# Kernel optimization log

Hardware: AMD Instinct MI355X
Metric: run time of the kernel (lower is better)

## Reference

```python
import jax, jax.numpy as jnp
import numpy as np

DN = ('NCHW', 'OIHW', 'NCHW')

def conv2d(x, w, b, stride, pad):
    y = jax.lax.conv_general_dilated(x, w, (stride, stride), [(pad, pad), (pad, pad)], dimension_numbers=DN)
    return y + b[None, :, None, None]

def conv_transpose2d(x, w, b):
    # torch ConvTranspose2d(k=4, stride=2, padding=1): out = (H-1)*2 - 2 + 4 = 2H
    # implemented as input-dilated conv with padding k-1-p = 2 on each side
    y = jax.lax.conv_general_dilated(x, w, (1, 1), [(2, 2), (2, 2)], lhs_dilation=(2, 2), dimension_numbers=DN)
    return y + b[None, :, None, None]

def setup_inputs() -> dict:
    key = jax.random.key(0)
    ks = jax.random.split(key, 8)
    K, D = 512, 128
    x = jax.random.normal(ks[0], (32, 3, 128, 128), jnp.float32)
    ew1 = jax.random.normal(ks[1], (128, 3, 4, 4), jnp.float32) * (1.0 / np.sqrt(3 * 16))
    eb1 = jnp.zeros((128,), jnp.float32)
    ew2 = jax.random.normal(ks[2], (D, 128, 4, 4), jnp.float32) * (1.0 / np.sqrt(128 * 16))
    eb2 = jnp.zeros((D,), jnp.float32)
    E = jax.random.uniform(ks[3], (K, D), jnp.float32, minval=-1.0 / K, maxval=1.0 / K)
    dw1 = jax.random.normal(ks[4], (128, D, 4, 4), jnp.float32) * (1.0 / np.sqrt(D * 16))
    db1 = jnp.zeros((128,), jnp.float32)
    dw2 = jax.random.normal(ks[5], (3, 128, 4, 4), jnp.float32) * (1.0 / np.sqrt(128 * 16))
    db2 = jnp.zeros((3,), jnp.float32)
    return {"x": x, "ew1": ew1, "eb1": eb1, "ew2": ew2, "eb2": eb2, "E": E,
            "dw1": dw1, "db1": db1, "dw2": dw2, "db2": db2}

def reference(x, ew1, eb1, ew2, eb2, E, dw1, db1, dw2, db2):
    # --- encoder: conv stack ---
    h = jax.nn.relu(conv2d(x, ew1, eb1, stride=2, pad=1))       # [B,128,64,64]
    z = conv2d(h, ew2, eb2, stride=2, pad=1)                    # [B,D,32,32] encoder_output
    B, C, H, W = z.shape
    Ze = jnp.transpose(z, (0, 2, 3, 1)).reshape(-1, C)          # [N_e, D], BHWC flattening
    # --- VQ: pairwise sq-dist, argmin, codebook lookup (== one-hot matmul in original) ---
    d = (jnp.sum(Ze * Ze, axis=1, keepdims=True)
         + jnp.sum(E * E, axis=1)
         - 2.0 * jnp.matmul(Ze, E.T))                           # [N_e, K]
    idx = jnp.argmin(d, axis=1)                                 # [N_e]
    Zq = E[idx]                                                 # [N_e, D]
    # faithful to original: Zq_mat.view(encoder_output.shape) with NO permute back
    dec_in = Zq.reshape(B, C, H, W)
    # straight-through estimator
    dec_in = z + jax.lax.stop_gradient(dec_in - z)
    # --- decoder: transposed conv stack ---
    g = jax.nn.relu(conv_transpose2d(dec_in, dw1, db1))         # [B,128,64,64]
    x_recon = jax.nn.sigmoid(conv_transpose2d(g, dw2, db2))     # [B,3,128,128]
    return x_recon
```

## Files before the change

### kernel.cpp

```cpp
#include <hip/hip_runtime.h>
#include <hip/hip_bf16.h>
#include <math.h>


typedef __attribute__((ext_vector_type(8))) short bf16x8;
typedef __attribute__((ext_vector_type(4))) float f32x4;

__device__ __forceinline__ void gload16(const void* g, const void* l) {
    __builtin_amdgcn_global_load_lds(
        (const __attribute__((address_space(1))) void*)g,
        (__attribute__((address_space(3))) void*)l, 16, 0, 0);
}

__device__ __forceinline__ int fragoff(int row, int ks, int lane) {
    return (row << 8) + (((ks << 6) + (lane & 0x30)) ^ ((row & 7) << 4));
}
__device__ __forceinline__ int fragoff64(int row, int ks, int lane) {
    return (row << 7) + (((ks << 6) + (lane & 0x30)) ^ ((row & 7) << 4));
}

__global__ __launch_bounds__(256) void k_init(
    const float* __restrict__ ew1, const float* __restrict__ ew2,
    const float* __restrict__ E,   const float* __restrict__ dw1,
    const float* __restrict__ dw2,
    __hip_bfloat16* __restrict__ hb,  __hip_bfloat16* __restrict__ w2p,
    __hip_bfloat16* __restrict__ w1p, __hip_bfloat16* __restrict__ Ep,
    __hip_bfloat16* __restrict__ w1b, __hip_bfloat16* __restrict__ w2db9,
    __hip_bfloat16* __restrict__ dq,  float* __restrict__ s2)
{
    int bid = blockIdx.x, t = threadIdx.x;
    bf16x8 zero8 = {0, 0, 0, 0, 0, 0, 0, 0};
    if (bid < 520) {
        int vid = bid * 256 + t;
        const int NROWV = 67584;
        if (vid < NROWV) {
            int c8 = (vid & 15) << 3;
            int xx = (vid >> 4) % 66;
            int r2 = vid / (66 * 16);
            int yy = (r2 & 1) * 65;
            int n = r2 >> 1;
            *(bf16x8*)&hb[((n * 66 + yy) * 66 + xx) * 128 + c8] = zero8;
        } else {
            int v2 = vid - NROWV;
            int c8 = (v2 & 15) << 3;
            int xs = (v2 >> 4) & 1;
            int yy = ((v2 >> 5) & 63) + 1;
            int n = v2 >> 11;
            *(bf16x8*)&hb[((n * 66 + yy) * 66 + xs * 65) * 128 + c8] = zero8;
        }
    } else if (bid < 1544) {
        int tid = (bid - 520) * 256 + t;
        int c = tid & 127, o = (tid >> 7) & 127, rs = tid >> 14;
        int r = rs >> 2, s = rs & 3;
        w2p[tid] = __float2bfloat16(ew2[((o * 128 + c) * 4 + r) * 4 + s]);
    } else if (bid < 2568) {
        int tid = (bid - 1544) * 256 + t;
        int c = tid & 127, o = (tid >> 7) & 127, m = tid >> 14;
        int pe = (m >> 3) & 1, qe = (m >> 2) & 1, tt = (m >> 1) & 1, u = m & 1;
        w1p[tid] = __float2bfloat16(dw1[((o * 128 + c) * 4 + (pe + 2 * tt)) * 4 + (qe + 2 * u)]);
    } else if (bid < 2824) {
        int tid = (bid - 2568) * 256 + t;
        Ep[tid] = __float2bfloat16(E[tid]);
    } else if (bid < 2856) {
        int tid = (bid - 2824) * 256 + t;
        int o = tid >> 6, cpos = tid & 63;
        int slot = cpos >> 3, e = cpos & 7;
        int k = ((slot ^ (o & 7)) << 3) | e;
        float v = 0.f;
        if (k < 48) {
            int c = k >> 4, r = (k >> 2) & 3, s = k & 3;
            v = ew1[((o * 3 + c) * 4 + r) * 4 + s];
        }
        w1b[tid] = __float2bfloat16(v);
    } else if (bid < 2928) {
        int tid = (bid - 2856) * 256 + t;
        int c = tid & 127;
        int col = (tid >> 7) & 15;
        int de = tid >> 11;
        int o = col & 3, pq = col >> 2;
        int d = de / 3, e_ = de - d * 3;
        int pe = pq >> 1, qe = pq & 1;
        int tt = d - pe, u = e_ - qe;
        float v = 0.f;
        if (o < 3 && tt >= 0 && tt < 2 && u >= 0 && u < 2)
            v = dw2[((o * 128 + c) * 4 + (pe + 2 * tt)) * 4 + (qe + 2 * u)];
        w2db9[tid] = __float2bfloat16(v);
    } else if (bid < 2930) {
        int k = (bid - 2928) * 256 + t;
        float a = 0.f;
        const float* e = E + k * 128;
        for (int c = 0; c < 128; ++c) a = fmaf(e[c], e[c], a);
        s2[k] = a;
    } else {
        int vid = (bid - 2930) * 256 + t;
        int n = vid / 2112;
        int rem = vid - n * 2112;
        int c8 = (rem & 15) << 3;
        int pp = rem >> 4;
        int yy, xx;
        if (pp < 68) { yy = (pp >= 34) ? 33 : 0; xx = pp % 34; }
        else { int q = pp - 68; yy = 1 + (q >> 1); xx = (q & 1) * 33; }
        *(bf16x8*)&dq[((n * 34 + yy) * 34 + xx) * 128 + c8] = zero8;
    }
}

__global__ __launch_bounds__(256) void k_conv1g(
    const float* __restrict__ x, const __hip_bfloat16* __restrict__ w1b,
    const float* __restrict__ b1, __hip_bfloat16* __restrict__ hb)
{
    __shared__ char smem[41984];
    int t = threadIdx.x, lane = t & 63, w = t >> 6;
    int wr = w >> 1, wc = w & 1;
    int bid0 = blockIdx.x;
    int bid = ((bid0 & 7) << 7) | (bid0 >> 3);
    int posbase = bid << 7;
    int ng = posbase >> 12, p0g = (posbase >> 6) & 63;

    #pragma unroll
    for (int i = 0; i < 4; ++i)
        gload16(w1b + ((w * 4 + i) * 512 + lane * 8), &smem[16384 + ((w * 4 + i) << 10)]);

    #pragma unroll
    for (int k3 = 0; k3 < 3; ++k3) {
        int j = w + (k3 << 2);
        if (j < 9) {
            int wrow = (j << 1) | (lane >> 5);
            int c = wrow / 6, yy = wrow - c * 6;
            int y = 2 * p0g - 1 + yy;
            int ysrc = y < 0 ? 0 : (y > 127 ? 127 : y);
            gload16(x + (((ng * 3 + c) * 128 + ysrc) << 7) + ((lane & 31) << 2),
                    &smem[32768 + (j << 10)]);
        }
    }
    __syncthreads();

    {
        int row = t >> 1, half = t & 1;
        int pl = row >> 6, q = row & 63;
        #pragma unroll
        for (int j = 0; j < 4; ++j) {
            int d = half * 4 + j;
            int sct = d ^ (row & 7);
            __hip_bfloat16 hv[8];
            #pragma unroll
            for (int e = 0; e < 8; ++e) {
                int k = sct * 8 + e;
                float v = 0.f;
                if (k < 48) {
                    int c = k >> 4, r = (k >> 2) & 3, s4 = k & 3;
                    int y = 2 * (p0g + pl) + r - 1;
                    int xg = 2 * q + s4 - 1;
                    if (((unsigned)y < 128u) && ((unsigned)xg < 128u)) {
                        int wrow = c * 6 + 2 * pl + r;
                        v = *(const float*)&smem[32768 + (wrow << 9) + (xg << 2)];
                    }
                }
                hv[e] = __float2bfloat16(v);
            }
            *(bf16x8*)&smem[(row << 7) + d * 16] = *(bf16x8*)hv;
        }
    }
    __syncthreads();

    f32x4 acc[4][4];
    #pragma unroll
    for (int mi = 0; mi < 4; ++mi)
        #pragma unroll
        for (int ni = 0; ni < 4; ++ni) acc[mi][ni] = (f32x4){0.f, 0.f, 0.f, 0.f};

    #pragma unroll
    for (int ks = 0; ks < 2; ++ks) {
        bf16x8 av[4], bv[4];
        #pragma unroll
        for (int mi = 0; mi < 4; ++mi)
            av[mi] = *(const bf16x8*)&smem[fragoff64((wr << 6) + (mi << 4) + (lane & 15), ks, lane)];
        #pragma unroll
        for (int ni = 0; ni < 4; ++ni)
            bv[ni] = *(const bf16x8*)&smem[16384 + fragoff64((wc << 6) + (ni << 4) + (lane & 15), ks, lane)];
        #pragma unroll
        for (int mi = 0; mi < 4; ++mi)
            #pragma unroll
            for (int ni = 0; ni < 4; ++ni)
                acc[mi][ni] = __builtin_amdgcn_mfma_f32_16x16x32_bf16(av[mi], bv[ni], acc[mi][ni], 0, 0, 0);
    }

    int rg = (lane >> 4) << 2;
    #pragma unroll
    for (int mi = 0; mi < 4; ++mi)
        #pragma unroll
        for (int ni = 0; ni < 4; ++ni) {
            int o = (wc << 6) + (ni << 4) + (lane & 15);
            float bias = b1[o];
            #pragma unroll
            for (int j = 0; j < 4; ++j) {
                int rowg = posbase + (wr << 6) + (mi << 4) + rg + j;
                int n = rowg >> 12, p = (rowg >> 6) & 63, q = rowg & 63;
                float v = acc[mi][ni][j] + bias;
                v = v > 0.f ? v : 0.f;
                hb[((n * 66 + p + 1) * 66 + q + 1) * 128 + o] = __float2bfloat16(v);
            }
        }
}

__global__ __launch_bounds__(256) void k_conv2vq(
    const __hip_bfloat16* __restrict__ hb, const __hip_bfloat16* __restrict__ w2p,
    const float* __restrict__ b2, const __hip_bfloat16* __restrict__ Ep,
    const float* __restrict__ s2, __hip_bfloat16* __restrict__ dq)
{
    __shared__ char smem[49152];
    int t = threadIdx.x, lane = t & 63, w = t >> 6;
    int bid0 = blockIdx.x;
    int bid = ((bid0 & 7) << 6) | (bid0 >> 3);
    int posbase = bid << 6;
    int n = posbase >> 10, p0 = (posbase >> 5) & 31;

    int aoff[2];
    #pragma unroll
    for (int i = 0; i < 2; ++i) {
        int r = ((w << 1) + i) * 8 + (lane >> 3);
        int slot = lane & 7;
        int p = p0 + (r >> 5), q = r & 31;
        aoff[i] = (((n * 66 + 2 * p) * 66 + 2 * q) << 7) + ((slot ^ (r & 7)) << 3);
    }
    int boff[4];
    #pragma unroll
    for (int i = 0; i < 4; ++i) {
        int o = ((w << 2) + i) * 8 + (lane >> 3);
        int slot = lane & 7;
        boff[i] = (o << 7) + ((slot ^ (o & 7)) << 3);
    }

#define C2_STAGE(STEP, BASE) { \
    int rs_ = (STEP) >> 1, ch_ = (STEP) & 1; \
    int aadd_ = ((((rs_ >> 2) * 66) + (rs_ & 3)) << 7) + (ch_ << 6); \
    int badd_ = (rs_ << 14) + (ch_ << 6); \
    _Pragma("unroll") \
    for (int i = 0; i < 2; ++i) \
        gload16(hb + aoff[i] + aadd_, &smem[(BASE) + (((w << 1) + i) << 10)]); \
    _Pragma("unroll") \
    for (int i = 0; i < 4; ++i) \
        gload16(w2p + boff[i] + badd_, &smem[(BASE) + 8192 + (((w << 2) + i) << 10)]); }

    f32x4 acc[4][2];
    #pragma unroll
    for (int mi = 0; mi < 4; ++mi)
        #pragma unroll
        for (int ni = 0; ni < 2; ++ni) acc[mi][ni] = (f32x4){0.f, 0.f, 0.f, 0.f};

    C2_STAGE(0, 0);
    __syncthreads();
    for (int step = 0; step < 32; ++step) {
        int cb = (step & 1) * 24576;
        if (step < 31) C2_STAGE(step + 1, ((step + 1) & 1) * 24576);
        #pragma unroll
        for (int ks = 0; ks < 2; ++ks) {
            bf16x8 av[4], bv[2];
            #pragma unroll
            for (int mi = 0; mi < 4; ++mi)
                av[mi] = *(const bf16x8*)&smem[cb + fragoff64((mi << 4) + (lane & 15), ks, lane)];
            #pragma unroll
            for (int ni = 0; ni < 2; ++ni)
                bv[ni] = *(const bf16x8*)&smem[cb + 8192 + fragoff64((w << 5) + (ni << 4) + (lane & 15), ks, lane)];
            #pragma unroll
            for (int mi = 0; mi < 4; ++mi)
                #pragma unroll
                for (int ni = 0; ni < 2; ++ni)
                    acc[mi][ni] = __builtin_amdgcn_mfma_f32_16x16x32_bf16(av[mi], bv[ni], acc[mi][ni], 0, 0, 0);
        }
        __syncthreads();
    }

#define VQ_STAGE(CHUNK, BASE) { \
    _Pragma("unroll") \
    for (int i = 0; i < 4; ++i) { \
        int kl_ = (((w << 2) + i) << 2) + (lane >> 4); \
        gload16(Ep + ((((CHUNK) << 6) + kl_) << 7) + (((lane & 15) ^ (kl_ & 7)) << 3), \
                &smem[(BASE) + (((w << 2) + i) << 10)]); \
    } }

    {
        int rg = (lane >> 4) << 2;
        #pragma unroll
        for (int mi = 0; mi < 4; ++mi)
            #pragma unroll
            for (int ni = 0; ni < 2; ++ni) {
                int o = (w << 5) + (ni << 4) + (lane & 15);
                float bias = b2[o];
                #pragma unroll
                for (int j = 0; j < 4; ++j) {
                    int r = (mi << 4) + rg + j;
                    int byteoff = (r << 8) + (((((o >> 3) ^ (r & 7))) << 4) | ((o & 7) << 1));
                    __hip_bfloat16 hv = __float2bfloat16(acc[mi][ni][j] + bias);
                    *(__hip_bfloat16*)&smem[byteoff] = hv;
                }
            }
    }
    VQ_STAGE(0, 16384);
    __syncthreads();

    float bvv[4][4];
    int   bii[4][4];
    #pragma unroll
    for (int mi = 0; mi < 4; ++mi)
        #pragma unroll
        for (int j = 0; j < 4; ++j) { bvv[mi][j] = 3.4e38f; bii[mi][j] = 0; }

    for (int chunk = 0; chunk < 8; ++chunk) {
        int eb = 16384 + ((chunk & 1) << 14);
        if (chunk < 7) VQ_STAGE(chunk + 1, 16384 + (((chunk + 1) & 1) << 14));
        f32x4 a2[4];
        #pragma unroll
        for (int mi = 0; mi < 4; ++mi) a2[mi] = (f32x4){0.f, 0.f, 0.f, 0.f};
        #pragma unroll
        for (int ks = 0; ks < 4; ++ks) {
            bf16x8 av[4], bv;
            #pragma unroll
            for (int mi = 0; mi < 4; ++mi)
                av[mi] = *(const bf16x8*)&smem[fragoff((mi << 4) + (lane & 15), ks, lane)];
            bv = *(const bf16x8*)&smem[eb + fragoff((w << 4) + (lane & 15), ks, lane)];
            #pragma unroll
            for (int mi = 0; mi < 4; ++mi)
                a2[mi] = __builtin_amdgcn_mfma_f32_16x16x32_bf16(av[mi], bv, a2[mi], 0, 0, 0);
        }
        int kg = (chunk << 6) + (w << 4) + (lane & 15);
        float s2v = s2[kg];
        #pragma unroll
        for (int mi = 0; mi < 4; ++mi)
            #pragma unroll
            for (int j = 0; j < 4; ++j) {
                float sc = s2v - 2.f * a2[mi][j];
                if (sc < bvv[mi][j]) { bvv[mi][j] = sc; bii[mi][j] = kg; }
            }
        __syncthreads();
    }

    float* redv  = (float*)&smem[16384];
    int*   redi  = (int*)&smem[16384 + 1024];
    int*   idx_l = (int*)&smem[16384 + 2048];
    #pragma unroll
    for (int mi = 0; mi < 4; ++mi)
        #pragma unroll
        for (int j = 0; j < 4; ++j) {
            float v = bvv[mi][j];
            int   ix = bii[mi][j];
            #pragma unroll
            for (int m = 1; m < 16; m <<= 1) {
                float ov = __shfl_xor(v, m, 64);
                int   oi = __shfl_xor(ix, m, 64);
                if (ov < v || (ov == v && oi < ix)) { v = ov; ix = oi; }
            }
            if ((lane & 15) == 0) {
                int r = (mi << 4) + ((lane >> 4) << 2) + j;
                redv[(r << 2) + w] = v;
                redi[(r << 2) + w] = ix;
            }
        }
    __syncthreads();
    if (t < 64) {
        float bv_ = redv[t << 2];
        int   bi_ = redi[t << 2];
        #pragma unroll
        for (int w2 = 1; w2 < 4; ++w2) {
            float ov = redv[(t << 2) + w2];
            int   oi = redi[(t << 2) + w2];
            if (ov < bv_ || (ov == bv_ && oi < bi_)) { bv_ = ov; bi_ = oi; }
        }
        idx_l[t] = bi_;
    }
    __syncthreads();

    #pragma unroll
    for (int i = 0; i < 4; ++i) {
        int idx2 = (w << 2) + i;
        int r = (idx2 << 2) + (lane >> 4);
        int krow = idx_l[r];
        gload16(Ep + ((krow << 7) + ((lane & 15) << 3)), &smem[idx2 << 10]);
    }
    __syncthreads();

    int cd0 = (posbase >> 3) & 127;
    const unsigned short* eb2p = (const unsigned short*)smem;
    #pragma unroll
    for (int k2 = 0; k2 < 4; ++k2) {
        int sp = (k2 << 8) + t;
        int hi = sp >> 7, lo = sp & 127;
        int y = sp >> 5, xx = sp & 31;
        unsigned short vals[8];
        #pragma unroll
        for (int ci = 0; ci < 8; ++ci)
            vals[ci] = eb2p[(((ci << 3) + hi) << 7) + lo];
        __hip_bfloat16* dst = dq + ((n * 34 + y + 1) * 34 + (xx + 1)) * 128 + cd0;
        *(bf16x8*)dst = *(bf16x8*)vals;
    }
}

__global__ __launch_bounds__(256) void k_deconv1(
    const __hip_bfloat16* __restrict__ dq, const __hip_bfloat16* __restrict__ w1p,
    const float* __restrict__ b1, __hip_bfloat16* __restrict__ g)
{
    __shared__ char smem[65536];
    int t = threadIdx.x, lane = t & 63, w = t >> 6;
    int wr = w >> 1, wc = w & 1;
    int bid0 = blockIdx.x;
    int bid = ((bid0 & 7) << 7) | (bid0 >> 3);
    int ag = bid & 7, qe = (bid >> 3) & 1, pe = (bid >> 4) & 1, n = bid >> 5;

    int aoff[4], boff[4];
    #pragma unroll
    for (int i = 0; i < 4; ++i) {
        int r = ((w << 2) + i) * 8 + (lane >> 3);
        int slot = lane & 7;
        int a = (ag << 2) + (r >> 5), b = r & 31;
        aoff[i] = (((n * 34 + (a + pe)) * 34 + (b + qe)) << 7) + ((slot ^ (r & 7)) << 3);
        boff[i] = (r << 7) + ((slot ^ (r & 7)) << 3);
    }
    int mbase = (pe << 3) | (qe << 2);

#define D1_STAGE(STEP, BASE) { \
    int tu_ = (STEP) >> 1, ch_ = (STEP) & 1; \
    int tt_ = tu_ >> 1, u_ = tu_ & 1; \
    int aadd_ = ((tt_ * 34 + u_) << 7) + (ch_ << 6); \
    int badd_ = ((mbase + tu_) << 14) + (ch_ << 6); \
    _Pragma("unroll") \
    for (int i = 0; i < 4; ++i) { \
        gload16(dq + aoff[i] + aadd_, &smem[(BASE) + (((w << 2) + i) << 10)]); \
        gload16(w1p + boff[i] + badd_, &smem[(BASE) + 16384 + (((w << 2) + i) << 10)]); \
    } }

    f32x4 acc[4][4];
    #pragma unroll
    for (int mi = 0; mi < 4; ++mi)
        #pragma unroll
        for (int ni = 0; ni < 4; ++ni) acc[mi][ni] = (f32x4){0.f, 0.f, 0.f, 0.f};

    D1_STAGE(0, 0);
    __syncthreads();
    for (int step = 0; step < 8; ++step) {
        int cb = (step & 1) * 32768;
        if (step < 7) D1_STAGE(step + 1, ((step + 1) & 1) * 32768);
        #pragma unroll
        for (int ks = 0; ks < 2; ++ks) {
            bf16x8 av[4], bv[4];
            #pragma unroll
            for (int mi = 0; mi < 4; ++mi)
                av[mi] = *(const bf16x8*)&smem[cb + fragoff64((wr << 6) + (mi << 4) + (lane & 15), ks, lane)];
            #pragma unroll
            for (int ni = 0; ni < 4; ++ni)
                bv[ni] = *(const bf16x8*)&smem[cb + 16384 + fragoff64((wc << 6) + (ni << 4) + (lane & 15), ks, lane)];
            #pragma unroll
            for (int mi = 0; mi < 4; ++mi)
                #pragma unroll
                for (int ni = 0; ni < 4; ++ni)
                    acc[mi][ni] = __builtin_amdgcn_mfma_f32_16x16x32_bf16(av[mi], bv[ni], acc[mi][ni], 0, 0, 0);
        }
        __syncthreads();
    }

    int rg = (lane >> 4) << 2;
    #pragma unroll
    for (int mi = 0; mi < 4; ++mi)
        #pragma unroll
        for (int ni = 0; ni < 4; ++ni) {
            int o = (wc << 6) + (ni << 4) + (lane & 15);
            float bias = b1[o];
            #pragma unroll
            for (int j = 0; j < 4; ++j) {
                int row = (wr << 6) + (mi << 4) + rg + j;
                int a = (ag << 2) + (row >> 5), b = row & 31;
                int y = 2 * a + pe, xx2 = 2 * b + qe;
                float v = acc[mi][ni][j] + bias;
                v = v > 0.f ? v : 0.f;
                g[((n * 66 + y + 1) * 66 + xx2 + 1) * 128 + o] = __float2bfloat16(v);
            }
        }
}

__global__ __launch_bounds__(256) void k_deconv2g(
    const __hip_bfloat16* __restrict__ g, const __hip_bfloat16* __restrict__ w2db9,
    const float* __restrict__ b2, float* __restrict__ out)
{
    __shared__ char smem[36864];
    int t = threadIdx.x, lane = t & 63, w = t >> 6;
    int bid0 = blockIdx.x;
    int bid = ((bid0 & 7) << 7) | (bid0 >> 3);
    int atile = bid & 31, n = bid >> 5;
    int a0 = atile << 1;

    int aoff[4];
    #pragma unroll
    for (int i = 0; i < 4; ++i) {
        int r = ((w << 2) + i) * 8 + (lane >> 3);
        int al = r >> 6, b = r & 63;
        aoff[i] = (((n * 66 + (a0 + al)) * 66 + b) << 7) + (((lane & 7) ^ (r & 7)) << 3);
    }

#define D2_STAGE(STEP, BASE) { \
    int de_ = (STEP) >> 1, ch_ = (STEP) & 1; \
    int dy_ = de_ / 3, dx_ = de_ - dy_ * 3; \
    int aadd_ = ((dy_ * 66 + dx_) << 7) + (ch_ << 6); \
    _Pragma("unroll") \
    for (int i = 0; i < 4; ++i) \
        gload16(g + aoff[i] + aadd_, &smem[(BASE) + (((w << 2) + i) << 10)]); \
    if (w < 2) { \
        int kl_ = (w << 3) + (lane >> 3); \
        gload16(w2db9 + (de_ << 11) + (kl_ << 7) + (ch_ << 6) + (((lane & 7) ^ (kl_ & 7)) << 3), \
                &smem[(BASE) + 16384 + (w << 10)]); \
    } }

    f32x4 acc[2];
    acc[0] = (f32x4){0.f, 0.f, 0.f, 0.f};
    acc[1] = (f32x4){0.f, 0.f, 0.f, 0.f};

    D2_STAGE(0, 0);
    __syncthreads();
    for (int step = 0; step < 18; ++step) {
        int cb = (step & 1) * 18432;
        if (step < 17) D2_STAGE(step + 1, ((step + 1) & 1) * 18432);
        #pragma unroll
        for (int ks = 0; ks < 2; ++ks) {
            bf16x8 av[2], bv;
            #pragma unroll
            for (int mi = 0; mi < 2; ++mi)
                av[mi] = *(const bf16x8*)&smem[cb + fragoff64((w << 5) + (mi << 4) + (lane & 15), ks, lane)];
            bv = *(const bf16x8*)&smem[cb + 16384 + fragoff64(lane & 15, ks, lane)];
            #pragma unroll
            for (int mi = 0; mi < 2; ++mi)
                acc[mi] = __builtin_amdgcn_mfma_f32_16x16x32_bf16(av[mi], bv, acc[mi], 0, 0, 0);
        }
        __syncthreads();
    }

    int rg = (lane >> 4) << 2;
    int col = lane & 15, o = col & 3, pq = col >> 2;
    if (o < 3) {
        int pe = pq >> 1, qe = pq & 1;
        float bias = b2[o];
        #pragma unroll
        for (int mi = 0; mi < 2; ++mi)
            #pragma unroll
            for (int j = 0; j < 4; ++j) {
                int row = (w << 5) + (mi << 4) + rg + j;
                int y = 2 * (a0 + (row >> 6)) + pe;
                int x = 2 * (row & 63) + qe;
                float v = acc[mi][j] + bias;
                out[((n * 3 + o) * 128 + y) * 128 + x] = 1.f / (1.f + expf(-v));
            }
    }
}

extern "C" void kernel_launch(void* const* d_in, const int* in_sizes, int n_in,
                              void* d_out, int out_size, void* d_ws, size_t ws_size,
                              hipStream_t stream) {
    const float* x   = (const float*)d_in[0];
    const float* ew1 = (const float*)d_in[1];
    const float* eb1 = (const float*)d_in[2];
    const float* ew2 = (const float*)d_in[3];
    const float* eb2 = (const float*)d_in[4];
    const float* E   = (const float*)d_in[5];
    const float* dw1 = (const float*)d_in[6];
    const float* db1 = (const float*)d_in[7];
    const float* dw2 = (const float*)d_in[8];
    const float* db2 = (const float*)d_in[9];
    float* out = (float*)d_out;

    char* W = (char*)d_ws;
    __hip_bfloat16* hb    = (__hip_bfloat16*)(W + 0);
    __hip_bfloat16* g     = (__hip_bfloat16*)(W + 0);
    __hip_bfloat16* dq    = (__hip_bfloat16*)(W + 75497472);
    __hip_bfloat16* w2p   = (__hip_bfloat16*)(W + 84967424);
    __hip_bfloat16* w1p   = (__hip_bfloat16*)(W + 85491712);
    __hip_bfloat16* Ep    = (__hip_bfloat16*)(W + 86016000);
    __hip_bfloat16* w2db9 = (__hip_bfloat16*)(W + 86147072);
    float*          s2    = (float*)(W + 86184192);
    __hip_bfloat16* w1b   = (__hip_bfloat16*)(W + 86186240);

    k_init    <<<3194, 256, 0, stream>>>(ew1, ew2, E, dw1, dw2,
                                         hb, w2p, w1p, Ep, w1b, w2db9, dq, s2);
    k_conv1g  <<<1024, 256, 0, stream>>>(x, w1b, eb1, hb);
    k_conv2vq <<<512,  256, 0, stream>>>(hb, w2p, eb2, Ep, s2, dq);
    k_deconv1 <<<1024, 256, 0, stream>>>(dq, w1p, db1, g);
    k_deconv2g<<<1024, 256, 0, stream>>>(g, w2db9, db2, out);
}
```

Before: 112.0 us.

## Double conv2+VQ tile to 128 positions with 512-thread blocks

The fused conv2+VQ kernel now processes 128 spatial positions per block with 8 waves arranged 2x4, in place of 64 positions with 4 waves. Each weight tile and codebook chunk loaded into LDS is therefore reused across twice as many rows, which halves global weight and codebook traffic per position and halves the block count. In exchange the kernel uses 64KB of LDS per block, which can lower occupancy, and with only 256 blocks the grid may leave part of the device idle. The dq write-out is restructured to emit two 16-byte stores per thread.

```diff
diff --git a/kernel.cpp b/kernel.cpp
--- a/kernel.cpp
+++ b/kernel.cpp
@@ -202,32 +202,28 @@
         }
 }
 
-__global__ __launch_bounds__(256) void k_conv2vq(
+__global__ __launch_bounds__(512) void k_conv2vq(
     const __hip_bfloat16* __restrict__ hb, const __hip_bfloat16* __restrict__ w2p,
     const float* __restrict__ b2, const __hip_bfloat16* __restrict__ Ep,
     const float* __restrict__ s2, __hip_bfloat16* __restrict__ dq)
 {
-    __shared__ char smem[49152];
+    __shared__ char smem[65536];
     int t = threadIdx.x, lane = t & 63, w = t >> 6;
+    int wr = w >> 2, wc = w & 3;
     int bid0 = blockIdx.x;
-    int bid = ((bid0 & 7) << 6) | (bid0 >> 3);
-    int posbase = bid << 6;
+    int bid = ((bid0 & 7) << 5) | (bid0 >> 3);
+    int posbase = bid << 7;
     int n = posbase >> 10, p0 = (posbase >> 5) & 31;
 
-    int aoff[2];
+    int aoff[2], boff[2];
     #pragma unroll
     for (int i = 0; i < 2; ++i) {
         int r = ((w << 1) + i) * 8 + (lane >> 3);
         int slot = lane & 7;
         int p = p0 + (r >> 5), q = r & 31;
-        aoff[i] = (((n * 66 + 2 * p) * 66 + 2 * q) << 7) + ((slot ^ (r & 7)) << 3);
-    }
-    int boff[4];
-    #pragma unroll
-    for (int i = 0; i < 4; ++i) {
-        int o = ((w << 2) + i) * 8 + (lane >> 3);
-        int slot = lane & 7;
-        boff[i] = (o << 7) + ((slot ^ (o & 7)) << 3);
+        int csw = (slot ^ (r & 7)) << 3;
+        aoff[i] = (((n * 66 + 2 * p) * 66 + 2 * q) << 7) + csw;
+        boff[i] = (r << 7) + csw;
     }
 
 #define C2_STAGE(STEP, BASE) { \
@@ -235,11 +231,10 @@
     int aadd_ = ((((rs_ >> 2) * 66) + (rs_ & 3)) << 7) + (ch_ << 6); \
     int badd_ = (rs_ << 14) + (ch_ << 6); \
     _Pragma("unroll") \
-    for (int i = 0; i < 2; ++i) \
+    for (int i = 0; i < 2; ++i) { \
         gload16(hb + aoff[i] + aadd_, &smem[(BASE) + (((w << 1) + i) << 10)]); \
-    _Pragma("unroll") \
-    for (int i = 0; i < 4; ++i) \
-        gload16(w2p + boff[i] + badd_, &smem[(BASE) + 8192 + (((w << 2) + i) << 10)]); }
+        gload16(w2p + boff[i] + badd_, &smem[(BASE) + 16384 + (((w << 1) + i) << 10)]); \
+    } }
 
     f32x4 acc[4][2];
     #pragma unroll
@@ -250,17 +245,17 @@
     C2_STAGE(0, 0);
     __syncthreads();
     for (int step = 0; step < 32; ++step) {
-        int cb = (step & 1) * 24576;
-        if (step < 31) C2_STAGE(step + 1, ((step + 1) & 1) * 24576);
+        int cb = (step & 1) * 32768;
+        if (step < 31) C2_STAGE(step + 1, ((step + 1) & 1) * 32768);
         #pragma unroll
         for (int ks = 0; ks < 2; ++ks) {
             bf16x8 av[4], bv[2];
             #pragma unroll
             for (int mi = 0; mi < 4; ++mi)
-                av[mi] = *(const bf16x8*)&smem[cb + fragoff64((mi << 4) + (lane & 15), ks, lane)];
+                av[mi] = *(const bf16x8*)&smem[cb + fragoff64((wr << 6) + (mi << 4) + (lane & 15), ks, lane)];
             #pragma unroll
             for (int ni = 0; ni < 2; ++ni)
-                bv[ni] = *(const bf16x8*)&smem[cb + 8192 + fragoff64((w << 5) + (ni << 4) + (lane & 15), ks, lane)];
+                bv[ni] = *(const bf16x8*)&smem[cb + 16384 + fragoff64((wc << 5) + (ni << 4) + (lane & 15), ks, lane)];
             #pragma unroll
             for (int mi = 0; mi < 4; ++mi)
                 #pragma unroll
@@ -272,10 +267,10 @@
 
 #define VQ_STAGE(CHUNK, BASE) { \
     _Pragma("unroll") \
-    for (int i = 0; i < 4; ++i) { \
-        int kl_ = (((w << 2) + i) << 2) + (lane >> 4); \
+    for (int i = 0; i < 2; ++i) { \
+        int kl_ = (((w << 1) + i) << 2) + (lane >> 4); \
         gload16(Ep + ((((CHUNK) << 6) + kl_) << 7) + (((lane & 15) ^ (kl_ & 7)) << 3), \
-                &smem[(BASE) + (((w << 2) + i) << 10)]); \
+                &smem[(BASE) + (((w << 1) + i) << 10)]); \
     } }
 
     {
@@ -284,18 +279,18 @@
         for (int mi = 0; mi < 4; ++mi)
             #pragma unroll
             for (int ni = 0; ni < 2; ++ni) {
-                int o = (w << 5) + (ni << 4) + (lane & 15);
+                int o = (wc << 5) + (ni << 4) + (lane & 15);
                 float bias = b2[o];
                 #pragma unroll
                 for (int j = 0; j < 4; ++j) {
-                    int r = (mi << 4) + rg + j;
+                    int r = (wr << 6) + (mi << 4) + rg + j;
                     int byteoff = (r << 8) + (((((o >> 3) ^ (r & 7))) << 4) | ((o & 7) << 1));
                     __hip_bfloat16 hv = __float2bfloat16(acc[mi][ni][j] + bias);
                     *(__hip_bfloat16*)&smem[byteoff] = hv;
                 }
             }
     }
-    VQ_STAGE(0, 16384);
+    VQ_STAGE(0, 32768);
     __syncthreads();
 
     float bvv[4][4];
@@ -306,23 +301,21 @@
         for (int j = 0; j < 4; ++j) { bvv[mi][j] = 3.4e38f; bii[mi][j] = 0; }
 
     for (int chunk = 0; chunk < 8; ++chunk) {
-        int eb = 16384 + ((chunk & 1) << 14);
-        if (chunk < 7) VQ_STAGE(chunk + 1, 16384 + (((chunk + 1) & 1) << 14));
+        int eb = 32768 + ((chunk & 1) << 14);
+        if (chunk < 7) VQ_STAGE(chunk + 1, 32768 + (((chunk + 1) & 1) << 14));
         f32x4 a2[4];
         #pragma unroll
         for (int mi = 0; mi < 4; ++mi) a2[mi] = (f32x4){0.f, 0.f, 0.f, 0.f};
         #pragma unroll
         for (int ks = 0; ks < 4; ++ks) {
-            bf16x8 av[4], bv;
-            #pragma unroll
-            for (int mi = 0; mi < 4; ++mi)
-                av[mi] = *(const bf16x8*)&smem[fragoff((mi << 4) + (lane & 15), ks, lane)];
-            bv = *(const bf16x8*)&smem[eb + fragoff((w << 4) + (lane & 15), ks, lane)];
-            #pragma unroll
-            for (int mi = 0; mi < 4; ++mi)
-                a2[mi] = __builtin_amdgcn_mfma_f32_16x16x32_bf16(av[mi], bv, a2[mi], 0, 0, 0);
-        }
-        int kg = (chunk << 6) + (w << 4) + (lane & 15);
+            bf16x8 bv = *(const bf16x8*)&smem[eb + fragoff((wc << 4) + (lane & 15), ks, lane)];
+            #pragma unroll
+            for (int mi = 0; mi < 4; ++mi) {
+                bf16x8 av = *(const bf16x8*)&smem[fragoff((wr << 6) + (mi << 4) + (lane & 15), ks, lane)];
+                a2[mi] = __builtin_amdgcn_mfma_f32_16x16x32_bf16(av, bv, a2[mi], 0, 0, 0);
+            }
+        }
+        int kg = (chunk << 6) + (wc << 4) + (lane & 15);
         float s2v = s2[kg];
         #pragma unroll
         for (int mi = 0; mi < 4; ++mi)
@@ -334,9 +327,9 @@
         __syncthreads();
     }
 
-    float* redv  = (float*)&smem[16384];
-    int*   redi  = (int*)&smem[16384 + 1024];
-    int*   idx_l = (int*)&smem[16384 + 2048];
+    float* redv  = (float*)&smem[32768];
+    int*   redi  = (int*)&smem[32768 + 2048];
+    int*   idx_l = (int*)&smem[32768 + 4096];
     #pragma unroll
     for (int mi = 0; mi < 4; ++mi)
         #pragma unroll
@@ -350,13 +343,13 @@
                 if (ov < v || (ov == v && oi < ix)) { v = ov; ix = oi; }
             }
             if ((lane & 15) == 0) {
-                int r = (mi << 4) + ((lane >> 4) << 2) + j;
-                redv[(r << 2) + w] = v;
-                redi[(r << 2) + w] = ix;
-            }
-        }
-    __syncthreads();
-    if (t < 64) {
+                int r = (wr << 6) + (mi << 4) + ((lane >> 4) << 2) + j;
+                redv[(r << 2) + wc] = v;
+                redi[(r << 2) + wc] = ix;
+            }
+        }
+    __syncthreads();
+    if (t < 128) {
         float bv_ = redv[t << 2];
         int   bi_ = redi[t << 2];
         #pragma unroll
@@ -381,16 +374,17 @@
     int cd0 = (posbase >> 3) & 127;
     const unsigned short* eb2p = (const unsigned short*)smem;
     #pragma unroll
-    for (int k2 = 0; k2 < 4; ++k2) {
-        int sp = (k2 << 8) + t;
+    for (int k2 = 0; k2 < 2; ++k2) {
+        int sp = (k2 << 9) + t;
         int hi = sp >> 7, lo = sp & 127;
-        int y = sp >> 5, xx = sp & 31;
-        unsigned short vals[8];
-        #pragma unroll
-        for (int ci = 0; ci < 8; ++ci)
-            vals[ci] = eb2p[(((ci << 3) + hi) << 7) + lo];
+        int y = hi * 4 + (lo >> 5), xx = lo & 31;
+        unsigned short vals[16];
+        #pragma unroll
+        for (int ci = 0; ci < 16; ++ci)
+            vals[ci] = eb2p[(((ci << 3) | hi) << 7) + lo];
         __hip_bfloat16* dst = dq + ((n * 34 + y + 1) * 34 + (xx + 1)) * 128 + cd0;
-        *(bf16x8*)dst = *(bf16x8*)vals;
+        *(bf16x8*)dst = *(bf16x8*)&vals[0];
+        *(bf16x8*)(dst + 8) = *(bf16x8*)&vals[8];
     }
 }
 
@@ -577,7 +571,7 @@
     k_init    <<<3194, 256, 0, stream>>>(ew1, ew2, E, dw1, dw2,
                                          hb, w2p, w1p, Ep, w1b, w2db9, dq, s2);
     k_conv1g  <<<1024, 256, 0, stream>>>(x, w1b, eb1, hb);
-    k_conv2vq <<<512,  256, 0, stream>>>(hb, w2p, eb2, Ep, s2, dq);
+    k_conv2vq <<<256,  512, 0, stream>>>(hb, w2p, eb2, Ep, s2, dq);
     k_deconv1 <<<1024, 256, 0, stream>>>(dq, w1p, db1, g);
     k_deconv2g<<<1024, 256, 0, stream>>>(g, w2db9, db2, out);
 }
```

Result: slower. 115.3 us (+2.9%).
